# Performance work log

Hardware: AMD Instinct MI355X
Metric: run time of the kernel (lower is better)

Reference implementation:

```python
import jax, jax.numpy as jnp
import numpy as np

B, DZ, DE, M, H = 4096, 2048, 128, 32, 1024
GATE_TEMP = 1.0


def setup_inputs() -> dict:
    key = jax.random.key(0)
    ks = jax.random.split(key, 6)
    s = lambda k, shape, sc: jax.random.normal(k, shape, dtype=jnp.float32) * sc
    return dict(
        z=s(ks[0], (B, DZ), 1.0),
        base_W=s(ks[1], (3, DZ), 0.02),
        base_b=jnp.zeros((3,), jnp.float32),
        gate_W=s(ks[2], (DE, DZ), 0.02),
        gate_b=jnp.zeros((DE,), jnp.float32),
        E=s(ks[3], (M, DE), 0.02),              # material embedding table
        W1=s(ks[4], (M, H, DZ + DE), 0.02),     # stacked first-layer weights
        b1=jnp.zeros((M, H), jnp.float32),
        W2=s(ks[5], (M, 3, H), 0.02),           # stacked second-layer weights
        b2=jnp.zeros((M, 3), jnp.float32),
    )


def _l2norm(x, eps=1e-12):
    # matches F.normalize(dim=-1): x / max(||x||_2, eps)
    n = jnp.linalg.norm(x, axis=-1, keepdims=True)
    return x / jnp.maximum(n, eps)


def reference(z, base_W, base_b, gate_W, gate_b, E, W1, b1, W2, b2):
    dz = z.shape[1]
    # base head: [B, 3]
    b = z @ base_W.T + base_b
    # gate similarities (routing logits): [B, M]
    q = _l2norm(z @ gate_W.T + gate_b)
    sims = q @ _l2norm(E).T
    # Per-material 2-layer MLP on cat([z, E_m]) fused as grouped GEMMs.
    # Split W1 into the z-part and embedding-part of the concat input.
    W1z, W1e = W1[:, :, :dz], W1[:, :, dz:]
    emb_term = jnp.einsum('me,mhe->mh', E, W1e)        # [M, H], shared across batch
    h = jax.nn.gelu(
        jnp.einsum('bi,mhi->bmh', z, W1z) + emb_term[None] + b1[None],
        approximate=False,
    )                                                   # [B, M, H]
    delta = jnp.einsum('bmh,moh->bmo', h, W2) + b2[None]  # [B, M, 3]
    # scale_delta_by_gate=False path; dropout inactive at inference.
    L = (b[:, None, :] + delta).reshape(z.shape[0], -1)   # [B, 3*M]
    return L, sims
```

## Files before the change

### kernel.cpp

```cpp
#include <hip/hip_runtime.h>
#include <hip/hip_bf16.h>
#include <math.h>

#define B_ROWS 4096
#define DZ     2048
#define DE     128
#define M_EXP  32
#define H_DIM  1024
#define NBIG   32768
#define NEXTRA 256
#define NTOT   (NBIG + NEXTRA)
#define W1_LD  (DZ + DE)

typedef _Float16 half8 __attribute__((ext_vector_type(8)));
typedef float    f32x4 __attribute__((ext_vector_type(4)));

#define AS1 __attribute__((address_space(1)))
#define AS3 __attribute__((address_space(3)))

__device__ __forceinline__ void async_copy16(const void* g, void* l) {
  __builtin_amdgcn_global_load_lds((const AS1 void*)g, (AS3 void*)l, 16, 0, 0);
}

__device__ __forceinline__ half8 cvt8(const float4& a, const float4& b) {
  half8 h = {(_Float16)a.x, (_Float16)a.y, (_Float16)a.z, (_Float16)a.w,
             (_Float16)b.x, (_Float16)b.y, (_Float16)b.z, (_Float16)b.w};
  return h;
}

__device__ __forceinline__ float gelu_f(float x) {
  float u = fabsf(x) * 0.70710678118654752f;
  float t = 1.0f / fmaf(0.3275911f, u, 1.0f);
  float poly = t * fmaf(t, fmaf(t, fmaf(t, fmaf(t, 1.061405429f, -1.453152027f),
                                        1.421413741f), -0.284496736f), 0.254829592f);
  float er = 1.0f - poly * __expf(-u * u);
  er = copysignf(er, x);
  return 0.5f * x * (1.0f + er);
}

__global__ __launch_bounds__(256) void k_cvt_z(const float* __restrict__ z,
                                               _Float16* __restrict__ zh) {
  long i = ((long)blockIdx.x * 256 + threadIdx.x) * 8;
  float4 a = *(const float4*)(z + i);
  float4 b = *(const float4*)(z + i + 4);
  *(half8*)(zh + i) = cvt8(a, b);
}

__global__ __launch_bounds__(256) void k_cvt_w1(const float* __restrict__ W1,
                                                const float* __restrict__ E,
                                                const float* __restrict__ b1,
                                                _Float16* __restrict__ W1h,
                                                float* __restrict__ hbias) {
  const long n = blockIdx.x;
  const int  t = threadIdx.x;
  const float* src = W1 + n * W1_LD;
  float4 a = *(const float4*)(src + t * 8);
  float4 b = *(const float4*)(src + t * 8 + 4);
  *(half8*)(W1h + n * DZ + t * 8) = cvt8(a, b);
  if (t < 32) {
    int m = (int)(n >> 10);
    float4 w = *(const float4*)(src + DZ + t * 4);
    float4 e = *(const float4*)(E + m * DE + t * 4);
    float p = w.x * e.x + w.y * e.y + w.z * e.z + w.w * e.w;
    p += __shfl_xor(p, 16);
    p += __shfl_xor(p, 8);
    p += __shfl_xor(p, 4);
    p += __shfl_xor(p, 2);
    p += __shfl_xor(p, 1);
    if (t == 0) hbias[n] = p + b1[n];
  }
}

__global__ __launch_bounds__(256) void k_cvt_small(const float* __restrict__ gate_W,
                                                   const float* __restrict__ base_W,
                                                   _Float16* __restrict__ W1h) {
  int r = blockIdx.x;
  int t = threadIdx.x;
  const float* src = nullptr;
  if (r < 128)       src = gate_W + (long)r * DZ;
  else if (r < 131)  src = base_W + (long)(r - 128) * DZ;
  _Float16* dst = W1h + (long)(NBIG + r) * DZ + t * 8;
  if (src) {
    float4 a = *(const float4*)(src + t * 8);
    float4 b = *(const float4*)(src + t * 8 + 4);
    *(half8*)dst = cvt8(a, b);
  } else {
    half8 zv = {(_Float16)0, (_Float16)0, (_Float16)0, (_Float16)0,
                (_Float16)0, (_Float16)0, (_Float16)0, (_Float16)0};
    *(half8*)dst = zv;
  }
}

__global__ __launch_bounds__(256, 2) void k_gemm(const _Float16* __restrict__ A,
                                                 const _Float16* __restrict__ Bm,
                                                 const float* __restrict__ hbias,
                                                 const float* __restrict__ W2,
                                                 float* __restrict__ Lout,
                                                 float* __restrict__ qraw) {
  __shared__ _Float16 sm[3][12288];

  int flat = blockIdx.y * gridDim.x + blockIdx.x;
  int wg   = (flat & 7) * 516 + (flat >> 3);
  const int tN = wg >> 5;
  const int tM = wg & 31;

  const int tid = threadIdx.x;
  const int w = tid >> 6, l = tid & 63;
  const int wm = w >> 1, wn = w & 1;
  const int rl = l & 15, lg = l >> 4;

  const int srow  = tid >> 2;
  const int sgoff = ((tid & 3) ^ ((srow >> 1) & 3)) * 8;
  const _Float16* gA = A  + (long)(tM * 128 + srow) * DZ + sgoff;
  const _Float16* gB = Bm + (long)(tN * 256 + srow) * DZ + sgoff;

#define STAGE_A(sb, kt) do { \
    async_copy16(gA + (kt) * 32,            &sm[sb][tid * 8]); \
    async_copy16(gA + 64 * DZ + (kt) * 32,  &sm[sb][2048 + tid * 8]); } while (0)
#define STAGE_B0(sb, kt) do { \
    async_copy16(gB + (kt) * 32,            &sm[sb][4096 + tid * 8]); \
    async_copy16(gB + 64 * DZ + (kt) * 32,  &sm[sb][6144 + tid * 8]); } while (0)
#define STAGE_B1(sb, kt) do { \
    async_copy16(gB + 128 * DZ + (kt) * 32, &sm[sb][8192 + tid * 8]); \
    async_copy16(gB + 192 * DZ + (kt) * 32, &sm[sb][10240 + tid * 8]); } while (0)

  const int aswz  = (lg ^ ((rl >> 1) & 3)) * 8;
  const int offA0 = (wm * 64 + rl) * 32 + aswz;
  const int offB0 = 4096 + (wn * 128 + rl) * 32 + aswz;

  half8 afE[4], afO[4], bf03[4], bf47[4];
  f32x4 acc[4][8];
  f32x4 z4 = {0.f, 0.f, 0.f, 0.f};
#pragma unroll
  for (int i = 0; i < 4; ++i)
#pragma unroll
    for (int j = 0; j < 8; ++j) acc[i][j] = z4;

#define RD_AF(dst, sl) do { _Pragma("unroll") for (int _i = 0; _i < 4; ++_i) \
    dst[_i] = *(const half8*)&sm[sl][offA0 + _i * 512]; } while (0)
#define RD_B03(sl) do { _Pragma("unroll") for (int _j = 0; _j < 4; ++_j) \
    bf03[_j] = *(const half8*)&sm[sl][offB0 + _j * 512]; } while (0)
#define RD_B47(sl) do { _Pragma("unroll") for (int _j = 0; _j < 4; ++_j) \
    bf47[_j] = *(const half8*)&sm[sl][offB0 + (4 + _j) * 512]; } while (0)

#define MFMA_J03(af_) do { __builtin_amdgcn_s_setprio(1); \
    _Pragma("unroll") for (int _i = 0; _i < 4; ++_i) \
    _Pragma("unroll") for (int _j = 0; _j < 4; ++_j) \
      acc[_i][_j] = __builtin_amdgcn_mfma_f32_16x16x32_f16(af_[_i], bf03[_j], acc[_i][_j], 0, 0, 0); \
    __builtin_amdgcn_s_setprio(0); } while (0)
#define MFMA_J47(af_) do { __builtin_amdgcn_s_setprio(1); \
    _Pragma("unroll") for (int _i = 0; _i < 4; ++_i) \
    _Pragma("unroll") for (int _j = 0; _j < 4; ++_j) \
      acc[_i][4 + _j] = __builtin_amdgcn_mfma_f32_16x16x32_f16(af_[_i], bf47[_j], acc[_i][4 + _j], 0, 0, 0); \
    __builtin_amdgcn_s_setprio(0); } while (0)

#define BAR() do { asm volatile("" ::: "memory"); __builtin_amdgcn_s_barrier(); asm volatile("" ::: "memory"); } while (0)
#define SBAR0 __builtin_amdgcn_sched_barrier(0)
#define VM6 asm volatile("s_waitcnt vmcnt(6)" ::: "memory")
#define VM0 asm volatile("s_waitcnt vmcnt(0)" ::: "memory")

#define PH_A(sl, sb, kt, AFc) do { \
    STAGE_A(sb, kt); STAGE_B0(sb, kt); BAR(); \
    RD_B47(sl); SBAR0; MFMA_J03(AFc); } while (0)
#define PH_A_N(sl, AFc) do { BAR(); \
    RD_B47(sl); SBAR0; MFMA_J03(AFc); } while (0)
#define PH_B(slN, sb, kt, AFc, AFn, CERT) do { \
    STAGE_B1(sb, kt); CERT; BAR(); \
    RD_AF(AFn, slN); RD_B03(slN); SBAR0; MFMA_J47(AFc); } while (0)
#define PH_B_N(slN, AFc, AFn, CERT) do { CERT; BAR(); \
    RD_AF(AFn, slN); RD_B03(slN); SBAR0; MFMA_J47(AFc); } while (0)
#define PH_B_LAST(AFc) do { BAR(); SBAR0; MFMA_J47(AFc); } while (0)

  STAGE_A(0, 0); STAGE_B0(0, 0); STAGE_B1(0, 0);
  STAGE_A(1, 1); STAGE_B0(1, 1); STAGE_B1(1, 1);
  VM6;
  BAR();
  RD_AF(afE, 0); RD_B03(0);

#pragma unroll 1
  for (int n = 0; n < 10; ++n) {
    const int t6 = 6 * n;
    PH_A(0, 2, t6 + 2, afE); PH_B(1, 2, t6 + 2, afE, afO, VM6);
    PH_A(1, 0, t6 + 3, afO); PH_B(2, 0, t6 + 3, afO, afE, VM6);
    PH_A(2, 1, t6 + 4, afE); PH_B(0, 1, t6 + 4, afE, afO, VM6);
    PH_A(0, 2, t6 + 5, afO); PH_B(1, 2, t6 + 5, afO, afE, VM6);
    PH_A(1, 0, t6 + 6, afE); PH_B(2, 0, t6 + 6, afE, afO, VM6);
    PH_A(2, 1, t6 + 7, afO); PH_B(0, 1, t6 + 7, afO, afE, VM6);
  }
  PH_A(0, 2, 62, afE); PH_B(1, 2, 62, afE, afO, VM6);
  PH_A(1, 0, 63, afO); PH_B(2, 0, 63, afO, afE, VM6);
  PH_A_N(2, afE);      PH_B_N(0, afE, afO, VM0);
  PH_A_N(0, afO);      PH_B_LAST(afO);

  if (tN < 128) {
    const int m = tN >> 2;
    float hb[8], w2v[3][8];
#pragma unroll
    for (int j = 0; j < 8; ++j) {
      int gcol = tN * 256 + wn * 128 + j * 16 + rl;
      int he   = gcol & (H_DIM - 1);
      hb[j] = hbias[gcol];
#pragma unroll
      for (int o = 0; o < 3; ++o) w2v[o][j] = W2[((long)m * 3 + o) * H_DIM + he];
    }
#pragma unroll
    for (int i = 0; i < 4; ++i) {
      const int growb = tM * 128 + wm * 64 + i * 16 + lg * 4;
#pragma unroll
      for (int r = 0; r < 4; ++r) {
        int grow = growb + r;
        float hv[8];
#pragma unroll
        for (int j = 0; j < 8; ++j) hv[j] = gelu_f(acc[i][j][r] + hb[j]);
#pragma unroll
        for (int o = 0; o < 3; ++o) {
          float p = 0.f;
#pragma unroll
          for (int j = 0; j < 8; ++j) p = fmaf(hv[j], w2v[o][j], p);
          p += __shfl_xor(p, 1);
          p += __shfl_xor(p, 2);
          p += __shfl_xor(p, 4);
          p += __shfl_xor(p, 8);
          if (rl == o) atomicAdd(&Lout[(long)grow * 96 + m * 3 + o], p);
        }
      }
    }
  } else {
#pragma unroll
    for (int i = 0; i < 4; ++i) {
      const int growb = tM * 128 + wm * 64 + i * 16 + lg * 4;
#pragma unroll
      for (int r = 0; r < 4; ++r) {
        int grow = growb + r;
        int c0 = wn * 128 + rl;
#pragma unroll
        for (int j = 0; j < 8; ++j)
          qraw[(long)grow * 256 + c0 + j * 16] = acc[i][j][r];
      }
    }
  }
}

__global__ __launch_bounds__(128) void k_post(const float* __restrict__ qraw,
                                              const float* __restrict__ gate_b,
                                              const float* __restrict__ base_b,
                                              const float* __restrict__ E,
                                              const float* __restrict__ b2,
                                              float* __restrict__ out) {
  const int b = blockIdx.x;
  const int t = threadIdx.x;
  __shared__ float qs[DE];
  __shared__ float invE[M_EXP];
  __shared__ float wsum[2];
  __shared__ float pA[M_EXP], pB[M_EXP];

  if (t < 32) {
    float ss = 0.f;
    const float* er = E + t * DE;
    for (int e = 0; e < DE; ++e) { float v = er[e]; ss += v * v; }
    invE[t] = 1.0f / fmaxf(sqrtf(ss), 1e-12f);
  }

  float val = qraw[(long)b * 256 + t] + gate_b[t];
  float ss = val * val;
  ss += __shfl_xor(ss, 1);  ss += __shfl_xor(ss, 2);  ss += __shfl_xor(ss, 4);
  ss += __shfl_xor(ss, 8);  ss += __shfl_xor(ss, 16); ss += __shfl_xor(ss, 32);
  if ((t & 63) == 0) wsum[t >> 6] = ss;
  __syncthreads();
  float inv = 1.0f / fmaxf(sqrtf(wsum[0] + wsum[1]), 1e-12f);
  qs[t] = val * inv;
  __syncthreads();

  {
    int m = t & 31, hf = t >> 5;
    const float* er = E + m * DE + hf * 32;
    const float* qq = qs + hf * 32;
    float p = 0.f;
#pragma unroll
    for (int e = 0; e < 32; ++e) p += qq[e] * er[e];
    p += __shfl_xor(p, 32);
    if (t < 32) pA[m] = p;
    else if (t >= 64 && t < 96) pB[m] = p;
    __syncthreads();
    if (t < 32) out[(long)B_ROWS * 96 + (long)b * 32 + t] = (pA[t] + pB[t]) * invE[t];
  }

  if (t < 96) {
    int o = t % 3;
    float bv = qraw[(long)b * 256 + 128 + o] + base_b[o];
    out[(long)b * 96 + t] += bv + b2[t];
  }
}

extern "C" void kernel_launch(void* const* d_in, const int* in_sizes, int n_in,
                              void* d_out, int out_size, void* d_ws, size_t ws_size,
                              hipStream_t stream) {
  const float* z      = (const float*)d_in[0];
  const float* base_W = (const float*)d_in[1];
  const float* base_b = (const float*)d_in[2];
  const float* gate_W = (const float*)d_in[3];
  const float* gate_b = (const float*)d_in[4];
  const float* E      = (const float*)d_in[5];
  const float* W1     = (const float*)d_in[6];
  const float* b1     = (const float*)d_in[7];
  const float* W2     = (const float*)d_in[8];
  const float* b2     = (const float*)d_in[9];
  float* out = (float*)d_out;

  char* ws = (char*)d_ws;
  const size_t off_zh    = 0;
  const size_t off_w1h   = off_zh  + (size_t)B_ROWS * DZ * 2;
  const size_t off_hbias = off_w1h + (size_t)NTOT * DZ * 2;
  const size_t off_qraw  = off_hbias + (size_t)NBIG * 4;
  _Float16* zh    = (_Float16*)(ws + off_zh);
  _Float16* W1h   = (_Float16*)(ws + off_w1h);
  float*    hbias = (float*)(ws + off_hbias);
  float*    qraw  = (float*)(ws + off_qraw);

  hipMemsetAsync(d_out, 0, (size_t)B_ROWS * 96 * sizeof(float), stream);

  k_cvt_z<<<(B_ROWS * DZ) / (256 * 8), 256, 0, stream>>>(z, zh);
  k_cvt_w1<<<NBIG, 256, 0, stream>>>(W1, E, b1, W1h, hbias);
  k_cvt_small<<<NEXTRA, 256, 0, stream>>>(gate_W, base_W, W1h);
  k_gemm<<<dim3(129, 32), 256, 0, stream>>>(zh, W1h, hbias, W2, out, qraw);
  k_post<<<B_ROWS, 128, 0, stream>>>(qraw, gate_b, base_b, E, b2, out);
}
```

Baseline: 784.5 us.

## Simplify GEMM main loop to one barrier per k-tile with full-tile LDS reads

Replaces the two-phase per-k-tile schedule, which used ping-pong A fragment registers, split B reads and sched_barriers, with a simpler loop. Each k-tile now does one barrier, reads all A/B fragments, issues the next stage's async copies, waits, and runs all 32 MFMAs. This halves the barrier count and frees one set of A-fragment registers. In exchange it loses the fine-grained interleaving of LDS reads with MFMAs and the compiler scheduling fences, so LDS latency may be exposed.

New measurement: 780.9 us. About the same (-0.5%).

```diff
diff --git a/kernel.cpp b/kernel.cpp
--- a/kernel.cpp
+++ b/kernel.cpp
@@ -128,7 +128,7 @@
   const int offA0 = (wm * 64 + rl) * 32 + aswz;
   const int offB0 = 4096 + (wn * 128 + rl) * 32 + aswz;
 
-  half8 afE[4], afO[4], bf03[4], bf47[4];
+  half8 af[4], bf03[4], bf47[4];
   f32x4 acc[4][8];
   f32x4 z4 = {0.f, 0.f, 0.f, 0.f};
 #pragma unroll
@@ -136,61 +136,55 @@
 #pragma unroll
     for (int j = 0; j < 8; ++j) acc[i][j] = z4;
 
-#define RD_AF(dst, sl) do { _Pragma("unroll") for (int _i = 0; _i < 4; ++_i) \
-    dst[_i] = *(const half8*)&sm[sl][offA0 + _i * 512]; } while (0)
+#define RD_AF(sl) do { _Pragma("unroll") for (int _i = 0; _i < 4; ++_i) \
+    af[_i] = *(const half8*)&sm[sl][offA0 + _i * 512]; } while (0)
 #define RD_B03(sl) do { _Pragma("unroll") for (int _j = 0; _j < 4; ++_j) \
     bf03[_j] = *(const half8*)&sm[sl][offB0 + _j * 512]; } while (0)
 #define RD_B47(sl) do { _Pragma("unroll") for (int _j = 0; _j < 4; ++_j) \
     bf47[_j] = *(const half8*)&sm[sl][offB0 + (4 + _j) * 512]; } while (0)
 
-#define MFMA_J03(af_) do { __builtin_amdgcn_s_setprio(1); \
+#define MFMA_J03() do { __builtin_amdgcn_s_setprio(1); \
     _Pragma("unroll") for (int _i = 0; _i < 4; ++_i) \
     _Pragma("unroll") for (int _j = 0; _j < 4; ++_j) \
-      acc[_i][_j] = __builtin_amdgcn_mfma_f32_16x16x32_f16(af_[_i], bf03[_j], acc[_i][_j], 0, 0, 0); \
+      acc[_i][_j] = __builtin_amdgcn_mfma_f32_16x16x32_f16(af[_i], bf03[_j], acc[_i][_j], 0, 0, 0); \
     __builtin_amdgcn_s_setprio(0); } while (0)
-#define MFMA_J47(af_) do { __builtin_amdgcn_s_setprio(1); \
+#define MFMA_J47() do { __builtin_amdgcn_s_setprio(1); \
     _Pragma("unroll") for (int _i = 0; _i < 4; ++_i) \
     _Pragma("unroll") for (int _j = 0; _j < 4; ++_j) \
-      acc[_i][4 + _j] = __builtin_amdgcn_mfma_f32_16x16x32_f16(af_[_i], bf47[_j], acc[_i][4 + _j], 0, 0, 0); \
+      acc[_i][4 + _j] = __builtin_amdgcn_mfma_f32_16x16x32_f16(af[_i], bf47[_j], acc[_i][4 + _j], 0, 0, 0); \
     __builtin_amdgcn_s_setprio(0); } while (0)
 
 #define BAR() do { asm volatile("" ::: "memory"); __builtin_amdgcn_s_barrier(); asm volatile("" ::: "memory"); } while (0)
-#define SBAR0 __builtin_amdgcn_sched_barrier(0)
 #define VM6 asm volatile("s_waitcnt vmcnt(6)" ::: "memory")
 #define VM0 asm volatile("s_waitcnt vmcnt(0)" ::: "memory")
 
-#define PH_A(sl, sb, kt, AFc) do { \
-    STAGE_A(sb, kt); STAGE_B0(sb, kt); BAR(); \
-    RD_B47(sl); SBAR0; MFMA_J03(AFc); } while (0)
-#define PH_A_N(sl, AFc) do { BAR(); \
-    RD_B47(sl); SBAR0; MFMA_J03(AFc); } while (0)
-#define PH_B(slN, sb, kt, AFc, AFn, CERT) do { \
-    STAGE_B1(sb, kt); CERT; BAR(); \
-    RD_AF(AFn, slN); RD_B03(slN); SBAR0; MFMA_J47(AFc); } while (0)
-#define PH_B_N(slN, AFc, AFn, CERT) do { CERT; BAR(); \
-    RD_AF(AFn, slN); RD_B03(slN); SBAR0; MFMA_J47(AFc); } while (0)
-#define PH_B_LAST(AFc) do { BAR(); SBAR0; MFMA_J47(AFc); } while (0)
+#define TILE_FULL(sl, s2, kt2) do { \
+    BAR(); \
+    RD_AF(sl); RD_B03(sl); RD_B47(sl); \
+    STAGE_A(s2, kt2); STAGE_B0(s2, kt2); STAGE_B1(s2, kt2); \
+    VM6; \
+    MFMA_J03(); MFMA_J47(); } while (0)
+#define TILE_NOST(sl, CERT) do { \
+    BAR(); \
+    RD_AF(sl); RD_B03(sl); RD_B47(sl); \
+    CERT; \
+    MFMA_J03(); MFMA_J47(); } while (0)
 
   STAGE_A(0, 0); STAGE_B0(0, 0); STAGE_B1(0, 0);
   STAGE_A(1, 1); STAGE_B0(1, 1); STAGE_B1(1, 1);
   VM6;
-  BAR();
-  RD_AF(afE, 0); RD_B03(0);
 
 #pragma unroll 1
-  for (int n = 0; n < 10; ++n) {
-    const int t6 = 6 * n;
-    PH_A(0, 2, t6 + 2, afE); PH_B(1, 2, t6 + 2, afE, afO, VM6);
-    PH_A(1, 0, t6 + 3, afO); PH_B(2, 0, t6 + 3, afO, afE, VM6);
-    PH_A(2, 1, t6 + 4, afE); PH_B(0, 1, t6 + 4, afE, afO, VM6);
-    PH_A(0, 2, t6 + 5, afO); PH_B(1, 2, t6 + 5, afO, afE, VM6);
-    PH_A(1, 0, t6 + 6, afE); PH_B(2, 0, t6 + 6, afE, afO, VM6);
-    PH_A(2, 1, t6 + 7, afO); PH_B(0, 1, t6 + 7, afO, afE, VM6);
-  }
-  PH_A(0, 2, 62, afE); PH_B(1, 2, 62, afE, afO, VM6);
-  PH_A(1, 0, 63, afO); PH_B(2, 0, 63, afO, afE, VM6);
-  PH_A_N(2, afE);      PH_B_N(0, afE, afO, VM0);
-  PH_A_N(0, afO);      PH_B_LAST(afO);
+  for (int n = 0; n < 20; ++n) {
+    const int t3 = 3 * n;
+    TILE_FULL(0, 2, t3 + 2);
+    TILE_FULL(1, 0, t3 + 3);
+    TILE_FULL(2, 1, t3 + 4);
+  }
+  TILE_FULL(0, 2, 62);
+  TILE_FULL(1, 0, 63);
+  TILE_NOST(2, VM0);
+  TILE_NOST(0, );
 
   if (tN < 128) {
     const int m = tN >> 2;
```
